# Performance work log

Hardware: AMD Instinct MI355X
Metric: run time of the kernel (lower is better)

The kernel has to match this reference:

```python
import jax, jax.numpy as jnp
import numpy as np

CUTOFFS = (2000, 20000, 50000)  # shortlist end, tail cluster boundaries; last == vocab
B, H, V = 8192, 1024, 50000
N_TAIL = len(CUTOFFS) - 1  # 2


def setup_inputs() -> dict:
    key = jax.random.key(0)
    ks = jax.random.split(key, 10)
    hidden = jax.random.normal(ks[0], (B, H), jnp.float32)
    targets = jax.random.randint(ks[1], (B,), 0, V, dtype=jnp.int64)
    embed_weight = jax.random.normal(ks[2], (V, H), jnp.float32) * 0.02
    # head: tail_vectors = nn.Linear(H, n_tail) -> W:(n_tail,H), b:(n_tail,)
    tail_vec_W = jax.random.normal(ks[3], (N_TAIL, H), jnp.float32) * 0.02
    tail_vec_b = jax.random.normal(ks[4], (N_TAIL,), jnp.float32) * 0.02
    shortlist_bias = jax.random.normal(ks[5], (CUTOFFS[0],), jnp.float32)
    bias0 = jax.random.normal(ks[6], (CUTOFFS[1] - CUTOFFS[0],), jnp.float32)
    bias1 = jax.random.normal(ks[7], (CUTOFFS[2] - CUTOFFS[1],), jnp.float32)
    # down_i = nn.Linear(H, H // 4**i, bias=False) -> W:(H//4**i, H)
    down0_W = jax.random.normal(ks[8], (H, H), jnp.float32) * (1.0 / np.sqrt(H))
    down1_W = jax.random.normal(ks[9], (H // 4, H), jnp.float32) * (1.0 / np.sqrt(H))
    return {
        "hidden": hidden, "embed_weight": embed_weight,
        "tail_vec_W": tail_vec_W, "tail_vec_b": tail_vec_b,
        "shortlist_bias": shortlist_bias, "bias0": bias0, "bias1": bias1,
        "down0_W": down0_W, "down1_W": down1_W, "targets": targets,
    }


def _cluster_ids(targets):
    # data-dependent sizes -> host-side index computation (matches torch nonzero)
    t = np.asarray(targets)
    ids = []
    for i in range(N_TAIL):
        ids.append(jnp.asarray(np.nonzero((t >= CUTOFFS[i]) & (t < CUTOFFS[i + 1]))[0]))
    return ids


def reference(hidden, embed_weight, tail_vec_W, tail_vec_b, shortlist_bias,
              bias0, bias1, down0_W, down1_W, targets):
    idx0, idx1 = _cluster_ids(targets)
    # head: shortlist logits + one logit per tail cluster
    shortlist = embed_weight[:CUTOFFS[0]]                       # (c0, H)
    head = jnp.concatenate(
        [hidden @ shortlist.T + shortlist_bias[None, :],         # (B, c0)
         hidden @ tail_vec_W.T + tail_vec_b[None, :]], axis=1)   # (B, n_tail)
    # tail cluster 0: down0 is H->H (reduce_factor**0 == 1, still applied)
    dec0 = embed_weight[CUTOFFS[0]:CUTOFFS[1]] @ down0_W.T       # (18000, H)
    out0 = (hidden[idx0] @ down0_W.T) @ dec0.T + bias0[None, :]  # (n0, 18000)
    # tail cluster 1: down1 is H -> H//4
    dec1 = embed_weight[CUTOFFS[1]:CUTOFFS[2]] @ down1_W.T       # (30000, 256)
    out1 = (hidden[idx1] @ down1_W.T) @ dec1.T + bias1[None, :]  # (n1, 30000)
    return (head, out0, out1)
```

## Files before the change

### kernel.cpp

```cpp
#include <hip/hip_runtime.h>
#include <hip/hip_bf16.h>

#define CUT0 2000
#define CUT1 20000
#define CUT2 50000
#define BSZ  8192
#define HDIM 1024
#define N0MAX 18000
#define N1MAX 30000
#define HEADW 2002

typedef __attribute__((ext_vector_type(8))) short bf16x8;
typedef __attribute__((ext_vector_type(4))) float f32x4;
typedef __attribute__((ext_vector_type(4))) unsigned short us4;

__device__ __forceinline__ unsigned short f2bf(float x) {
    unsigned u = __float_as_uint(x);
    unsigned r = u + 0x7fffu + ((u >> 16) & 1u);
    return (unsigned short)(r >> 16);
}

__device__ __forceinline__ bf16x8 pack8(f32x4 a, f32x4 b) {
    bf16x8 w;
    w[0] = (short)f2bf(a[0]); w[1] = (short)f2bf(a[1]);
    w[2] = (short)f2bf(a[2]); w[3] = (short)f2bf(a[3]);
    w[4] = (short)f2bf(b[0]); w[5] = (short)f2bf(b[1]);
    w[6] = (short)f2bf(b[2]); w[7] = (short)f2bf(b[3]);
    return w;
}

typedef const __attribute__((address_space(1))) void* gas_ptr;
typedef __attribute__((address_space(3))) void* las_ptr;

__device__ __forceinline__ void load_lds16(const void* g, void* l) {
    __builtin_amdgcn_global_load_lds((gas_ptr)g, (las_ptr)l, 16, 0, 0);
}

__global__ __launch_bounds__(1024) void build_idx(const int* __restrict__ targets,
                                                  int* __restrict__ n0,
                                                  int* __restrict__ n1,
                                                  int* __restrict__ idx0,
                                                  int* __restrict__ idx1) {
    __shared__ int s0[1024], s1[1024];
    const int t = threadIdx.x;
    const int base = t * 8;
    int tg[8];
    int c0 = 0, c1 = 0;
#pragma unroll
    for (int i = 0; i < 8; ++i) {
        tg[i] = targets[base + i];
        c0 += (tg[i] >= CUT0 && tg[i] < CUT1) ? 1 : 0;
        c1 += (tg[i] >= CUT1) ? 1 : 0;
    }
    s0[t] = c0; s1[t] = c1;
    __syncthreads();
    for (int off = 1; off < 1024; off <<= 1) {
        int v0 = 0, v1 = 0;
        if (t >= off) { v0 = s0[t - off]; v1 = s1[t - off]; }
        __syncthreads();
        s0[t] += v0; s1[t] += v1;
        __syncthreads();
    }
    int p0 = s0[t] - c0, p1 = s1[t] - c1;
#pragma unroll
    for (int i = 0; i < 8; ++i) {
        if (tg[i] >= CUT0 && tg[i] < CUT1)      idx0[p0++] = base + i;
        else if (tg[i] >= CUT1)                 idx1[p1++] = base + i;
    }
    if (t == 1023) { *n0 = s0[1023]; *n1 = s1[1023]; }
}

#define CVT_TOTAL 5738
__global__ __launch_bounds__(256) void cvt_all(
    const float* __restrict__ hidden, const float* __restrict__ embed,
    const float* __restrict__ tailW,  const float* __restrict__ down0,
    const float* __restrict__ down1,  const float* __restrict__ slbias,
    const float* __restrict__ tailb,
    unsigned short* __restrict__ hbf, unsigned short* __restrict__ ebf,
    unsigned short* __restrict__ d0bf, unsigned short* __restrict__ d1bf,
    float* __restrict__ bias2002)
{
    const int b = blockIdx.x;
    const float* src; unsigned short* dst; long long e;
    if (b < 4096)      { src = hidden; dst = hbf;  e = (long long)b * 2048; }
    else if (b < 5096) { src = embed;  dst = ebf;  e = (long long)(b - 4096) * 2048; }
    else if (b == 5096){ src = tailW;  dst = ebf + (size_t)CUT0 * HDIM; e = 0; }
    else if (b < 5609) { src = down0;  dst = d0bf; e = (long long)(b - 5097) * 2048; }
    else if (b < 5737) { src = down1;  dst = d1bf; e = (long long)(b - 5609) * 2048; }
    else {
        for (int j = threadIdx.x; j < HEADW; j += 256)
            bias2002[j] = (j < CUT0) ? slbias[j] : tailb[j - CUT0];
        return;
    }
    const long long i = e + (long long)threadIdx.x * 8;
    f32x4 a = *(const f32x4*)(src + i);
    f32x4 c = *(const f32x4*)(src + i + 4);
    us4 p = { f2bf(a[0]), f2bf(a[1]), f2bf(a[2]), f2bf(a[3]) };
    us4 q = { f2bf(c[0]), f2bf(c[1]), f2bf(c[2]), f2bf(c[3]) };
    *(us4*)(dst + i)     = p;
    *(us4*)(dst + i + 4) = q;
}

template<bool A_F32, bool SPLIT_GATHER, bool OUT_BF16, bool HAS_BIAS>
__device__ __forceinline__ void gemm_body(
    const void* __restrict__ Av, const float* __restrict__ AgF,
    const unsigned short* __restrict__ B,
    int gsplit, int gbase, const int* __restrict__ idxTail,
    int M, int N, int K,
    const float* __restrict__ bias,
    void* __restrict__ Cv, long long cbase, int ldC,
    int m0, int n0)
{
    __shared__ unsigned short As[4][8192];
    __shared__ unsigned short Bs[4][8192];

    const int tid  = threadIdx.x;
    const int wave = tid >> 6, lane = tid & 63;
    const int wr = wave >> 2;
    const int wc = wave & 3;
    const int lrow = lane & 15;
    const int quad = lane >> 4;

    const int srow = lane >> 2;
    const int scol = (((lane & 3) ^ ((srow >> 1) & 3)) << 3);
    int tr0 = wave * 32 + srow, tr1 = tr0 + 16;
    int bn0 = n0 + tr0; bn0 = bn0 < N ? bn0 : N - 1;
    int bn1 = n0 + tr1; bn1 = bn1 < N ? bn1 : N - 1;
    const unsigned short* bP0 = B + (long long)bn0 * K + scol;
    const unsigned short* bP1 = B + (long long)bn1 * K + scol;

    const unsigned short* aP0 = nullptr;
    const unsigned short* aP1 = nullptr;
    const float* aF = nullptr;
    int oA0 = 0, oA1 = 0, sA0 = 0, sA1 = 0;
    if constexpr (!A_F32) {
        int am0 = m0 + tr0; am0 = am0 < M ? am0 : M - 1;
        int am1 = m0 + tr1; am1 = am1 < M ? am1 : M - 1;
        long long ar0, ar1;
        if constexpr (SPLIT_GATHER) {
            ar0 = (am0 < gsplit) ? (long long)(gbase + am0) : (long long)idxTail[am0 - gsplit];
            ar1 = (am1 < gsplit) ? (long long)(gbase + am1) : (long long)idxTail[am1 - gsplit];
        } else { ar0 = am0; ar1 = am1; }
        const unsigned short* Ab = (const unsigned short*)Av;
        aP0 = Ab + ar0 * (long long)K + scol;
        aP1 = Ab + ar1 * (long long)K + scol;
    } else {
        const int rA  = lane >> 1;
        const int trA = wave * 32 + rA;
        int amF = m0 + trA; amF = amF < M ? amF : M - 1;
        long long rowi; const float* bp;
        if constexpr (SPLIT_GATHER) {
            if (amF < gsplit) { rowi = (long long)(gbase + amF); bp = (const float*)Av; }
            else              { rowi = (long long)idxTail[amF - gsplit]; bp = AgF; }
        } else { rowi = amF; bp = (const float*)Av; }
        aF  = bp + rowi * (long long)K;
        sA0 = (lane & 1);
        sA1 = 2 + (lane & 1);
        const int xA = (rA >> 1) & 3;
        oA0 = trA * 32 + ((sA0 ^ xA) << 3);
        oA1 = trA * 32 + ((sA1 ^ xA) << 3);
    }

    f32x4 acc[8][4];
#pragma unroll
    for (int i = 0; i < 8; ++i)
#pragma unroll
        for (int j = 0; j < 4; ++j) acc[i][j] = (f32x4){0.f, 0.f, 0.f, 0.f};

    const int KT = K >> 5;

    auto issueB = [&](int tt) {
        unsigned short* bs = &Bs[tt & 3][wave * 1024];
        load_lds16(bP0 + (tt << 5), bs);
        load_lds16(bP1 + (tt << 5), bs + 512);
    };
    auto issueA16 = [&](int tt) {
        unsigned short* as = &As[tt & 3][wave * 1024];
        load_lds16(aP0 + (tt << 5), as);
        load_lds16(aP1 + (tt << 5), as + 512);
    };

    const int npro = KT < 3 ? KT : 3;
    for (int tt = 0; tt < npro; ++tt) {
        issueB(tt);
        if constexpr (!A_F32) {
            issueA16(tt);
        } else {
            const float* p = aF + (tt << 5);
            f32x4 x0 = *(const f32x4*)(p + sA0 * 8);
            f32x4 x1 = *(const f32x4*)(p + sA0 * 8 + 4);
            f32x4 y0 = *(const f32x4*)(p + sA1 * 8);
            f32x4 y1 = *(const f32x4*)(p + sA1 * 8 + 4);
            *(bf16x8*)&As[tt & 3][oA0] = pack8(x0, x1);
            *(bf16x8*)&As[tt & 3][oA1] = pack8(y0, y1);
        }
    }
    if constexpr (A_F32)
        asm volatile("s_waitcnt lgkmcnt(0)" ::: "memory");

    const int rdswz = ((quad ^ ((lrow >> 1) & 3)) << 3);

    for (int t = 0; t < KT; ++t) {
        const int tt = t + 3;
        const bool pf = (tt < KT);

        f32x4 x0, x1, y0, y1;
        if constexpr (!A_F32) {
            if (pf) { issueB(tt); issueA16(tt); }
        } else {
            if (pf) {
                issueB(tt);
                const float* p = aF + (tt << 5);
                x0 = *(const f32x4*)(p + sA0 * 8);
                x1 = *(const f32x4*)(p + sA0 * 8 + 4);
                y0 = *(const f32x4*)(p + sA1 * 8);
                y1 = *(const f32x4*)(p + sA1 * 8 + 4);
            }
        }

        int infl = KT - 1 - t; if (infl > 3) infl = 3;
        if constexpr (!A_F32) {
            if (infl >= 3)      asm volatile("s_waitcnt vmcnt(12)" ::: "memory");
            else if (infl == 2) asm volatile("s_waitcnt vmcnt(8)"  ::: "memory");
            else if (infl == 1) asm volatile("s_waitcnt vmcnt(4)"  ::: "memory");
            else                asm volatile("s_waitcnt vmcnt(0)"  ::: "memory");
        } else {
            if (infl >= 3)      asm volatile("s_waitcnt vmcnt(10)" ::: "memory");
            else if (infl == 2) asm volatile("s_waitcnt vmcnt(4)"  ::: "memory");
            else if (infl == 1) asm volatile("s_waitcnt vmcnt(2)"  ::: "memory");
            else                asm volatile("s_waitcnt vmcnt(0)"  ::: "memory");
        }

        __builtin_amdgcn_s_barrier();
        asm volatile("" ::: "memory");

        const unsigned short* Asl = &As[t & 3][0];
        const unsigned short* Bsl = &Bs[t & 3][0];

        bf16x8 a[8], b[4];
#pragma unroll
        for (int mi = 0; mi < 8; ++mi) {
            const int R = wr * 128 + mi * 16 + lrow;
            a[mi] = *(const bf16x8*)&Asl[R * 32 + rdswz];
        }
#pragma unroll
        for (int nj = 0; nj < 4; ++nj) {
            const int R = wc * 64 + nj * 16 + lrow;
            b[nj] = *(const bf16x8*)&Bsl[R * 32 + rdswz];
        }

        __builtin_amdgcn_s_setprio(1);
#pragma unroll
        for (int mi = 0; mi < 8; ++mi)
#pragma unroll
            for (int nj = 0; nj < 4; ++nj)
                acc[mi][nj] = __builtin_amdgcn_mfma_f32_16x16x32_bf16(
                    a[mi], b[nj], acc[mi][nj], 0, 0, 0);
        __builtin_amdgcn_s_setprio(0);

        if constexpr (A_F32) {
            if (pf) {
                *(bf16x8*)&As[tt & 3][oA0] = pack8(x0, x1);
                *(bf16x8*)&As[tt & 3][oA1] = pack8(y0, y1);
            }
            asm volatile("s_waitcnt lgkmcnt(0)" ::: "memory");
        }

        asm volatile("" ::: "memory");
        __builtin_amdgcn_s_barrier();
    }

#pragma unroll
    for (int mi = 0; mi < 8; ++mi) {
#pragma unroll
        for (int v = 0; v < 4; ++v) {
            int m = m0 + wr * 128 + mi * 16 + quad * 4 + v;
            if (m >= M) continue;
#pragma unroll
            for (int nj = 0; nj < 4; ++nj) {
                int n = n0 + wc * 64 + nj * 16 + lrow;
                if (n >= N) continue;
                float r = acc[mi][nj][v];
                if constexpr (OUT_BF16) {
                    ((unsigned short*)Cv)[(long long)m * ldC + n] = f2bf(r);
                } else {
                    if constexpr (HAS_BIAS) r += bias[n];
                    ((float*)Cv)[cbase + (long long)m * ldC + n] = r;
                }
            }
        }
    }
}

__global__ __launch_bounds__(512) void gemm_head(
    const unsigned short* __restrict__ hbf, const unsigned short* __restrict__ ebf,
    const float* __restrict__ bias2002, float* __restrict__ out)
{
    gemm_body<false, false, false, true>(
        hbf, nullptr, ebf, 0, 0, nullptr,
        BSZ, HEADW, HDIM, bias2002, out, 0ll, HEADW,
        (int)blockIdx.y * 256, (int)blockIdx.x * 256);
}

__global__ __launch_bounds__(512) void gemm_c0c1(
    const float* __restrict__ embed, const float* __restrict__ hidden,
    const unsigned short* __restrict__ d0bf, const unsigned short* __restrict__ d1bf,
    const int* __restrict__ idx0, const int* __restrict__ idx1,
    const int* __restrict__ n0p, const int* __restrict__ n1p,
    unsigned short* __restrict__ c0, unsigned short* __restrict__ c1)
{
    int bx = blockIdx.x;
    const unsigned short* Bb; const int* idxT;
    int gsplit, gbase, M, N, ldC; unsigned short* C;
    if (bx < 4) {
        Bb = d0bf; idxT = idx0; gsplit = N0MAX; gbase = CUT0;
        M = N0MAX + *n0p; N = HDIM; ldC = HDIM; C = c0;
    } else {
        bx -= 4;
        Bb = d1bf; idxT = idx1; gsplit = N1MAX; gbase = CUT1;
        M = N1MAX + *n1p; N = 256; ldC = 256; C = c1;
    }
    const int m0 = (int)blockIdx.y * 256;
    const int n0 = bx * 256;
    if (m0 >= M) return;
    gemm_body<true, true, true, false>(
        embed, hidden, Bb, gsplit, gbase, idxT,
        M, N, HDIM, nullptr, C, 0ll, ldC, m0, n0);
}

__global__ __launch_bounds__(512) void gemm_out01(
    const unsigned short* __restrict__ c0, const unsigned short* __restrict__ c1,
    const int* __restrict__ n0p, const int* __restrict__ n1p,
    const float* __restrict__ bias0, const float* __restrict__ bias1,
    float* __restrict__ out)
{
    int bx = blockIdx.x;
    const unsigned short *A, *B; const float* bias;
    int M, N, K, ldC; long long cbase;
    if (bx < 71) {
        A = c0 + (size_t)N0MAX * HDIM; B = c0; bias = bias0;
        M = *n0p; N = N0MAX; K = HDIM; ldC = N0MAX;
        cbase = (long long)BSZ * HEADW;
    } else {
        bx -= 71;
        A = c1 + (size_t)N1MAX * 256; B = c1; bias = bias1;
        M = *n1p; N = N1MAX; K = 256; ldC = N1MAX;
        cbase = (long long)BSZ * HEADW + (long long)(*n0p) * N0MAX;
    }
    const int m0 = (int)blockIdx.y * 256;
    const int n0 = bx * 256;
    if (m0 >= M) return;
    gemm_body<false, false, false, true>(
        A, nullptr, B, 0, 0, nullptr,
        M, N, K, bias, out, cbase, ldC, m0, n0);
}

extern "C" void kernel_launch(void* const* d_in, const int* in_sizes, int n_in,
                              void* d_out, int out_size, void* d_ws, size_t ws_size,
                              hipStream_t stream) {
    (void)in_sizes; (void)n_in; (void)out_size; (void)ws_size;
    const float* hidden  = (const float*)d_in[0];
    const float* embed   = (const float*)d_in[1];
    const float* tailW   = (const float*)d_in[2];
    const float* tailb   = (const float*)d_in[3];
    const float* slbias  = (const float*)d_in[4];
    const float* bias0   = (const float*)d_in[5];
    const float* bias1   = (const float*)d_in[6];
    const float* down0   = (const float*)d_in[7];
    const float* down1   = (const float*)d_in[8];
    const int*   targets = (const int*)d_in[9];
    float* out = (float*)d_out;

    char* ws = (char*)d_ws;
    int* n0p  = (int*)ws;
    int* n1p  = n0p + 1;
    int* idx0 = (int*)(ws + 256);
    int* idx1 = idx0 + BSZ;
    size_t off = 256 + 2 * (size_t)BSZ * 4;
    unsigned short* hbf  = (unsigned short*)(ws + off); off += (size_t)BSZ * HDIM * 2;
    unsigned short* ebf  = (unsigned short*)(ws + off); off += (size_t)HEADW * HDIM * 2;
    float* bias2002      = (float*)(ws + off);          off += 2048 * 4;
    unsigned short* c0   = (unsigned short*)(ws + off);
    off += (size_t)(N0MAX + BSZ) * HDIM * 2;
    unsigned short* c1   = (unsigned short*)(ws + off);
    off += (size_t)(N1MAX + BSZ) * 256 * 2;
    unsigned short* d0bf = (unsigned short*)(ws + off); off += (size_t)HDIM * HDIM * 2;
    unsigned short* d1bf = (unsigned short*)(ws + off); off += (size_t)256 * HDIM * 2;

    build_idx<<<1, 1024, 0, stream>>>(targets, n0p, n1p, idx0, idx1);

    cvt_all<<<CVT_TOTAL, 256, 0, stream>>>(
        hidden, embed, tailW, down0, down1, slbias, tailb,
        hbf, ebf, d0bf, d1bf, bias2002);

    gemm_c0c1<<<dim3(5, 150), 512, 0, stream>>>(
        embed, hidden, d0bf, d1bf, idx0, idx1, n0p, n1p, c0, c1);

    gemm_head<<<dim3(8, 32), 512, 0, stream>>>(hbf, ebf, bias2002, out);

    gemm_out01<<<dim3(189, 32), 512, 0, stream>>>(
        c0, c1, n0p, n1p, bias0, bias1, out);
}
```

Measured before the change: 1.585 ms.

## Merge index build into convert kernel and fuse head GEMM with down-projections

Folds the target-index prefix scan into the conversion kernel as an extra block and drops the bf16 conversion of hidden. The head GEMM now reads fp32 hidden directly (A_F32 path) and runs in the same launch as the c0/c1 down-projection GEMMs, using a flattened 1D grid. Launch count drops from five to three, about 16 MB of hidden-conversion traffic disappears, and the head GEMM blocks can fill the GPU alongside the projection blocks. In exchange, the head GEMM converts fp32 to bf16 inside its load path, and shared memory is now declared per kernel and passed into the GEMM body.

```diff
diff --git a/kernel.cpp b/kernel.cpp
--- a/kernel.cpp
+++ b/kernel.cpp
@@ -36,62 +36,59 @@
     __builtin_amdgcn_global_load_lds((gas_ptr)g, (las_ptr)l, 16, 0, 0);
 }
 
-__global__ __launch_bounds__(1024) void build_idx(const int* __restrict__ targets,
-                                                  int* __restrict__ n0,
-                                                  int* __restrict__ n1,
-                                                  int* __restrict__ idx0,
-                                                  int* __restrict__ idx1) {
-    __shared__ int s0[1024], s1[1024];
-    const int t = threadIdx.x;
-    const int base = t * 8;
-    int tg[8];
-    int c0 = 0, c1 = 0;
-#pragma unroll
-    for (int i = 0; i < 8; ++i) {
-        tg[i] = targets[base + i];
-        c0 += (tg[i] >= CUT0 && tg[i] < CUT1) ? 1 : 0;
-        c1 += (tg[i] >= CUT1) ? 1 : 0;
-    }
-    s0[t] = c0; s1[t] = c1;
-    __syncthreads();
-    for (int off = 1; off < 1024; off <<= 1) {
-        int v0 = 0, v1 = 0;
-        if (t >= off) { v0 = s0[t - off]; v1 = s1[t - off]; }
-        __syncthreads();
-        s0[t] += v0; s1[t] += v1;
-        __syncthreads();
-    }
-    int p0 = s0[t] - c0, p1 = s1[t] - c1;
-#pragma unroll
-    for (int i = 0; i < 8; ++i) {
-        if (tg[i] >= CUT0 && tg[i] < CUT1)      idx0[p0++] = base + i;
-        else if (tg[i] >= CUT1)                 idx1[p1++] = base + i;
-    }
-    if (t == 1023) { *n0 = s0[1023]; *n1 = s1[1023]; }
-}
-
-#define CVT_TOTAL 5738
+#define CVT_NBLK 1643
 __global__ __launch_bounds__(256) void cvt_all(
-    const float* __restrict__ hidden, const float* __restrict__ embed,
-    const float* __restrict__ tailW,  const float* __restrict__ down0,
-    const float* __restrict__ down1,  const float* __restrict__ slbias,
-    const float* __restrict__ tailb,
-    unsigned short* __restrict__ hbf, unsigned short* __restrict__ ebf,
+    const float* __restrict__ embed,  const float* __restrict__ tailW,
+    const float* __restrict__ down0,  const float* __restrict__ down1,
+    const float* __restrict__ slbias, const float* __restrict__ tailb,
+    const int* __restrict__ targets,
+    unsigned short* __restrict__ ebf,
     unsigned short* __restrict__ d0bf, unsigned short* __restrict__ d1bf,
-    float* __restrict__ bias2002)
+    float* __restrict__ bias2002,
+    int* __restrict__ n0p, int* __restrict__ n1p,
+    int* __restrict__ idx0, int* __restrict__ idx1)
 {
     const int b = blockIdx.x;
-    const float* src; unsigned short* dst; long long e;
-    if (b < 4096)      { src = hidden; dst = hbf;  e = (long long)b * 2048; }
-    else if (b < 5096) { src = embed;  dst = ebf;  e = (long long)(b - 4096) * 2048; }
-    else if (b == 5096){ src = tailW;  dst = ebf + (size_t)CUT0 * HDIM; e = 0; }
-    else if (b < 5609) { src = down0;  dst = d0bf; e = (long long)(b - 5097) * 2048; }
-    else if (b < 5737) { src = down1;  dst = d1bf; e = (long long)(b - 5609) * 2048; }
-    else {
+    if (b == 1642) {
+        __shared__ int s0[256], s1[256];
+        const int t = threadIdx.x;
+        const int base = t * 32;
+        int tg[32];
+        int c0n = 0, c1n = 0;
+#pragma unroll
+        for (int i = 0; i < 32; ++i) {
+            tg[i] = targets[base + i];
+            c0n += (tg[i] >= CUT0 && tg[i] < CUT1) ? 1 : 0;
+            c1n += (tg[i] >= CUT1) ? 1 : 0;
+        }
+        s0[t] = c0n; s1[t] = c1n;
+        __syncthreads();
+        for (int o = 1; o < 256; o <<= 1) {
+            int v0 = 0, v1 = 0;
+            if (t >= o) { v0 = s0[t - o]; v1 = s1[t - o]; }
+            __syncthreads();
+            s0[t] += v0; s1[t] += v1;
+            __syncthreads();
+        }
+        int p0 = s0[t] - c0n, p1 = s1[t] - c1n;
+#pragma unroll
+        for (int i = 0; i < 32; ++i) {
+            if (tg[i] >= CUT0 && tg[i] < CUT1)      idx0[p0++] = base + i;
+            else if (tg[i] >= CUT1)                 idx1[p1++] = base + i;
+        }
+        if (t == 255) { *n0p = s0[255]; *n1p = s1[255]; }
+        return;
+    }
+    if (b == 1641) {
         for (int j = threadIdx.x; j < HEADW; j += 256)
             bias2002[j] = (j < CUT0) ? slbias[j] : tailb[j - CUT0];
         return;
     }
+    const float* src; unsigned short* dst; long long e;
+    if (b < 1000)      { src = embed; dst = ebf;  e = (long long)b * 2048; }
+    else if (b == 1000){ src = tailW; dst = ebf + (size_t)CUT0 * HDIM; e = 0; }
+    else if (b < 1513) { src = down0; dst = d0bf; e = (long long)(b - 1001) * 2048; }
+    else               { src = down1; dst = d1bf; e = (long long)(b - 1513) * 2048; }
     const long long i = e + (long long)threadIdx.x * 8;
     f32x4 a = *(const f32x4*)(src + i);
     f32x4 c = *(const f32x4*)(src + i + 4);
@@ -103,6 +100,8 @@
 
 template<bool A_F32, bool SPLIT_GATHER, bool OUT_BF16, bool HAS_BIAS>
 __device__ __forceinline__ void gemm_body(
+    unsigned short (* __restrict__ As)[8192],
+    unsigned short (* __restrict__ Bs)[8192],
     const void* __restrict__ Av, const float* __restrict__ AgF,
     const unsigned short* __restrict__ B,
     int gsplit, int gbase, const int* __restrict__ idxTail,
@@ -111,9 +110,6 @@
     void* __restrict__ Cv, long long cbase, int ldC,
     int m0, int n0)
 {
-    __shared__ unsigned short As[4][8192];
-    __shared__ unsigned short Bs[4][8192];
-
     const int tid  = threadIdx.x;
     const int wave = tid >> 6, lane = tid & 63;
     const int wr = wave >> 2;
@@ -292,40 +288,45 @@
     }
 }
 
-__global__ __launch_bounds__(512) void gemm_head(
-    const unsigned short* __restrict__ hbf, const unsigned short* __restrict__ ebf,
-    const float* __restrict__ bias2002, float* __restrict__ out)
-{
-    gemm_body<false, false, false, true>(
-        hbf, nullptr, ebf, 0, 0, nullptr,
-        BSZ, HEADW, HDIM, bias2002, out, 0ll, HEADW,
-        (int)blockIdx.y * 256, (int)blockIdx.x * 256);
-}
-
-__global__ __launch_bounds__(512) void gemm_c0c1(
-    const float* __restrict__ embed, const float* __restrict__ hidden,
+__global__ __launch_bounds__(512) void gemm_mid(
+    const float* __restrict__ hidden, const float* __restrict__ embed,
+    const unsigned short* __restrict__ ebf,
     const unsigned short* __restrict__ d0bf, const unsigned short* __restrict__ d1bf,
+    const float* __restrict__ bias2002,
     const int* __restrict__ idx0, const int* __restrict__ idx1,
     const int* __restrict__ n0p, const int* __restrict__ n1p,
+    float* __restrict__ out,
     unsigned short* __restrict__ c0, unsigned short* __restrict__ c1)
 {
-    int bx = blockIdx.x;
-    const unsigned short* Bb; const int* idxT;
-    int gsplit, gbase, M, N, ldC; unsigned short* C;
-    if (bx < 4) {
-        Bb = d0bf; idxT = idx0; gsplit = N0MAX; gbase = CUT0;
-        M = N0MAX + *n0p; N = HDIM; ldC = HDIM; C = c0;
-    } else {
-        bx -= 4;
-        Bb = d1bf; idxT = idx1; gsplit = N1MAX; gbase = CUT1;
-        M = N1MAX + *n1p; N = 256; ldC = 256; C = c1;
-    }
-    const int m0 = (int)blockIdx.y * 256;
-    const int n0 = bx * 256;
+    __shared__ unsigned short As[4][8192];
+    __shared__ unsigned short Bs[4][8192];
+    int id = blockIdx.x;
+    if (id < 256) {
+        const int bx = id & 7, by = id >> 3;
+        gemm_body<true, false, false, true>(
+            As, Bs, hidden, nullptr, ebf, 0, 0, nullptr,
+            BSZ, HEADW, HDIM, bias2002, out, 0ll, HEADW,
+            by * 256, bx * 256);
+        return;
+    }
+    id -= 256;
+    if (id < 4 * 103) {
+        const int bx = id & 3, by = id >> 2;
+        const int M = N0MAX + *n0p;
+        const int m0 = by * 256;
+        if (m0 >= M) return;
+        gemm_body<true, true, true, false>(
+            As, Bs, embed, hidden, d0bf, N0MAX, CUT0, idx0,
+            M, HDIM, HDIM, nullptr, c0, 0ll, HDIM, m0, bx * 256);
+        return;
+    }
+    id -= 412;
+    const int M = N1MAX + *n1p;
+    const int m0 = id * 256;
     if (m0 >= M) return;
     gemm_body<true, true, true, false>(
-        embed, hidden, Bb, gsplit, gbase, idxT,
-        M, N, HDIM, nullptr, C, 0ll, ldC, m0, n0);
+        As, Bs, embed, hidden, d1bf, N1MAX, CUT1, idx1,
+        M, 256, HDIM, nullptr, c1, 0ll, 256, m0, 0);
 }
 
 __global__ __launch_bounds__(512) void gemm_out01(
@@ -334,6 +335,8 @@
     const float* __restrict__ bias0, const float* __restrict__ bias1,
     float* __restrict__ out)
 {
+    __shared__ unsigned short As[4][8192];
+    __shared__ unsigned short Bs[4][8192];
     int bx = blockIdx.x;
     const unsigned short *A, *B; const float* bias;
     int M, N, K, ldC; long long cbase;
@@ -351,7 +354,7 @@
     const int n0 = bx * 256;
     if (m0 >= M) return;
     gemm_body<false, false, false, true>(
-        A, nullptr, B, 0, 0, nullptr,
+        As, Bs, A, nullptr, B, 0, 0, nullptr,
         M, N, K, bias, out, cbase, ldC, m0, n0);
 }
 
@@ -377,7 +380,6 @@
     int* idx0 = (int*)(ws + 256);
     int* idx1 = idx0 + BSZ;
     size_t off = 256 + 2 * (size_t)BSZ * 4;
-    unsigned short* hbf  = (unsigned short*)(ws + off); off += (size_t)BSZ * HDIM * 2;
     unsigned short* ebf  = (unsigned short*)(ws + off); off += (size_t)HEADW * HDIM * 2;
     float* bias2002      = (float*)(ws + off);          off += 2048 * 4;
     unsigned short* c0   = (unsigned short*)(ws + off);
@@ -387,16 +389,13 @@
     unsigned short* d0bf = (unsigned short*)(ws + off); off += (size_t)HDIM * HDIM * 2;
     unsigned short* d1bf = (unsigned short*)(ws + off); off += (size_t)256 * HDIM * 2;
 
-    build_idx<<<1, 1024, 0, stream>>>(targets, n0p, n1p, idx0, idx1);
-
-    cvt_all<<<CVT_TOTAL, 256, 0, stream>>>(
-        hidden, embed, tailW, down0, down1, slbias, tailb,
-        hbf, ebf, d0bf, d1bf, bias2002);
-
-    gemm_c0c1<<<dim3(5, 150), 512, 0, stream>>>(
-        embed, hidden, d0bf, d1bf, idx0, idx1, n0p, n1p, c0, c1);
-
-    gemm_head<<<dim3(8, 32), 512, 0, stream>>>(hbf, ebf, bias2002, out);
+    cvt_all<<<CVT_NBLK, 256, 0, stream>>>(
+        embed, tailW, down0, down1, slbias, tailb, targets,
+        ebf, d0bf, d1bf, bias2002, n0p, n1p, idx0, idx1);
+
+    gemm_mid<<<818, 512, 0, stream>>>(
+        hidden, embed, ebf, d0bf, d1bf, bias2002,
+        idx0, idx1, n0p, n1p, out, c0, c1);
 
     gemm_out01<<<dim3(189, 32), 512, 0, stream>>>(
         c0, c1, n0p, n1p, bias0, bias1, out);
```

New measurement: 1.565 ms. No clear change (-1.2%).
